# Kernel tuning notes

Measured on AMD Instinct MI355X. Metric: run time of the kernel, lower is better.

## Reference

```python
import jax, jax.numpy as jnp
import numpy as np

BN_EPS = 1e-5

def conv1d(x, w, b, pad):
    # x: (B, C_in, L), w: (C_out, C_in, K=4), stride 1
    y = jax.lax.conv_general_dilated(x, w, window_strides=(1,), padding=[(pad, pad)],
                                     dimension_numbers=('NCH', 'OIH', 'NCH'))
    return y + b[None, :, None]

def batchnorm_train(x, g, be):
    # training-mode BN over (N, L) per channel, biased variance (torch semantics)
    m = jnp.mean(x, axis=(0, 2), keepdims=True)
    v = jnp.mean((x - m) ** 2, axis=(0, 2), keepdims=True)
    return (x - m) * jax.lax.rsqrt(v + BN_EPS) * g[None, :, None] + be[None, :, None]

def setup_inputs() -> dict:
    key = jax.random.key(0)
    ks = jax.random.split(key, 12)
    B, T, C_in, E, K = 32, 4096, 12, 256, 1024
    d = {}
    d['x'] = jax.random.normal(ks[0], (B, T, C_in), jnp.float32)
    d['w1'] = jax.random.normal(ks[1], (E, C_in, 4), jnp.float32) * 0.1
    d['b1'] = jax.random.normal(ks[2], (E,), jnp.float32) * 0.1
    d['g1'] = jnp.ones((E,), jnp.float32); d['be1'] = jnp.zeros((E,), jnp.float32)
    d['w2'] = jax.random.normal(ks[3], (E, E, 4), jnp.float32) * 0.05
    d['b2'] = jax.random.normal(ks[4], (E,), jnp.float32) * 0.1
    d['g2'] = jnp.ones((E,), jnp.float32); d['be2'] = jnp.zeros((E,), jnp.float32)
    d['w3'] = jax.random.normal(ks[5], (E, E, 4), jnp.float32) * 0.05
    d['b3'] = jax.random.normal(ks[6], (E,), jnp.float32) * 0.1
    d['g3'] = jnp.ones((E,), jnp.float32); d['be3'] = jnp.zeros((E,), jnp.float32)
    d['w4'] = jax.random.normal(ks[7], (E, E, 4), jnp.float32) * 0.05
    d['b4'] = jax.random.normal(ks[8], (E,), jnp.float32) * 0.1
    d['codebook'] = jax.random.normal(ks[9], (K, E), jnp.float32)
    return d

def reference(x, w1, b1, g1, be1, w2, b2, g2, be2, w3, b3, g3, be3, w4, b4, codebook):
    h = jnp.transpose(x, (0, 2, 1))                 # (B, C, T)
    h = jax.nn.relu(batchnorm_train(conv1d(h, w1, b1, 2), g1, be1))  # (B,E,T+1)
    h = jax.nn.relu(batchnorm_train(conv1d(h, w2, b2, 1), g2, be2))  # (B,E,T)
    h = jax.nn.relu(batchnorm_train(conv1d(h, w3, b3, 2), g3, be3))  # (B,E,T+1)
    h = conv1d(h, w4, b4, 1)                                         # (B,E,T)
    z_e = jnp.transpose(h, (0, 2, 1))               # (B, T, E)
    # squared-L2 nearest codebook entry (argmin identical to cdist p=2)
    d2 = (jnp.sum(z_e ** 2, axis=-1, keepdims=True)
          - 2.0 * jnp.einsum('bte,ke->btk', z_e, codebook)
          + jnp.sum(codebook ** 2, axis=-1)[None, None, :])
    ids = jnp.argmin(d2, axis=-1)                   # (B, T) int
    z_q = codebook[ids]                             # gather (B, T, E)
    z_q = z_e + jax.lax.stop_gradient(z_q - z_e)    # straight-through
    return (z_e, z_q)
```

## Files before the change

kernel.cpp:

```cpp
#include <hip/hip_runtime.h>
#include <hip/hip_bf16.h>


#define B_   32
#define T_   4096
#define E_   256
#define CIN_ 12
#define LM_  4096

typedef __attribute__((ext_vector_type(4))) float f32x4;
typedef __attribute__((ext_vector_type(8))) short bf16x8;
typedef __attribute__((ext_vector_type(8))) unsigned short u16x8;

__device__ __forceinline__ unsigned int bf_rne(float v) {
  unsigned int u = __float_as_uint(v);
  return (u + 0x7fffu + ((u >> 16) & 1u)) >> 16;
}
__device__ __forceinline__ void split2(float v, unsigned short& h, unsigned short& l) {
  unsigned int hu = bf_rne(v);
  h = (unsigned short)hu;
  l = (unsigned short)bf_rne(v - __uint_as_float(hu << 16));
}
__device__ __forceinline__ void split3(float v, unsigned short& a,
                                       unsigned short& b, unsigned short& c) {
  unsigned int h = bf_rne(v);
  a = (unsigned short)h;
  float r1 = v - __uint_as_float(h << 16);
  unsigned int m = bf_rne(r1);
  b = (unsigned short)m;
  float r2 = r1 - __uint_as_float(m << 16);
  c = (unsigned short)bf_rne(r2);
}

__global__ __launch_bounds__(256) void prep_w_kernel(
    const float* __restrict__ w, unsigned short* __restrict__ wh,
    unsigned short* __restrict__ wm, unsigned short* __restrict__ wl) {
  const int g = blockIdx.x * 256 + threadIdx.x;
  const int coff  = g & 31;
  const int e     = (g >> 5) & 255;
  const int slice = g >> 13;
  const int cc = slice >> 2, kt = slice & 3;
  const int c = cc * 32 + coff;
  unsigned short h, m, l;
  split3(w[(size_t)e * 1024 + (size_t)c * 4 + kt], h, m, l);
  const size_t o = (size_t)slice * 8192 + (size_t)e * 32 + coff;
  wh[o] = h; wm[o] = m; wl[o] = l;
}

__global__ __launch_bounds__(256) void conv1_kernel(
    const float* __restrict__ x, const float* __restrict__ w1,
    const float* __restrict__ b1, float* __restrict__ out_main,
    float* __restrict__ out_tail) {
  __shared__ __align__(16) float xs[259][12];
  __shared__ __align__(16) float wsh[E_ * 48];
  __shared__ float bs[E_];
  const int tid = threadIdx.x;
  const int b = blockIdx.y;
  const int l0 = blockIdx.x * 256;
  for (int idx = tid; idx < 259 * 12; idx += 256) {
    int r = idx / 12, c = idx - r * 12;
    int t = l0 - 2 + r;
    xs[r][c] = (t >= 0 && t < T_) ? x[((size_t)b * T_ + t) * CIN_ + c] : 0.f;
  }
  for (int idx = tid; idx < E_ * 48; idx += 256) wsh[idx] = w1[idx];
  bs[tid] = b1[tid];
  __syncthreads();
  float xr[4][12];
  #pragma unroll
  for (int r = 0; r < 4; ++r)
    #pragma unroll
    for (int c = 0; c < 12; ++c) xr[r][c] = xs[tid + r][c];
  const int l = l0 + tid;
  for (int e = 0; e < E_; ++e) {
    float acc = bs[e];
    #pragma unroll
    for (int c = 0; c < 12; ++c) {
      const float4 wv = *(const float4*)&wsh[e * 48 + c * 4];
      acc += wv.x * xr[0][c] + wv.y * xr[1][c] + wv.z * xr[2][c] + wv.w * xr[3][c];
    }
    if (l < LM_)       out_main[((size_t)b * E_ + e) * LM_ + l] = acc;
    else if (l == LM_) out_tail[(size_t)b * E_ + e] = acc;
  }
}

__global__ __launch_bounds__(256) void bn_pass1(
    const float* __restrict__ hmain, const float* __restrict__ htail,
    float* __restrict__ psum, float* __restrict__ psq) {
  const int bx = blockIdx.x;
  const int c = bx >> 3, sl = bx & 7;
  const int tid = threadIdx.x;
  float s = 0.f, s2 = 0.f;
  for (int b = 0; b < B_; ++b) {
    const float* p = hmain + ((size_t)b * E_ + c) * LM_ + sl * 512;
    const float v0 = p[tid], v1 = p[tid + 256];
    s += v0 + v1;
    s2 += v0 * v0 + v1 * v1;
  }
  if (htail && sl == 7 && tid < B_) {
    const float v = htail[(size_t)tid * E_ + c];
    s += v; s2 += v * v;
  }
  __shared__ float sh[256], sh2[256];
  sh[tid] = s; sh2[tid] = s2; __syncthreads();
  for (int off = 128; off > 0; off >>= 1) {
    if (tid < off) { sh[tid] += sh[tid + off]; sh2[tid] += sh2[tid + off]; }
    __syncthreads();
  }
  if (tid == 0) { psum[bx] = sh[0]; psq[bx] = sh2[0]; }
}

__global__ __launch_bounds__(256) void bn_pass2(
    const float* __restrict__ psum, const float* __restrict__ psq,
    const float* __restrict__ g, const float* __restrict__ be,
    float* __restrict__ scale, float* __restrict__ shift, int hasTail) {
  const int c = threadIdx.x;
  double s = 0.0, s2 = 0.0;
  #pragma unroll
  for (int i = 0; i < 8; ++i) { s += psum[c * 8 + i]; s2 += psq[c * 8 + i]; }
  double N = (double)B_ * (double)(LM_ + hasTail);
  double m = s / N, var = s2 / N - m * m;
  double a = (double)g[c] / sqrt(var + 1e-5);
  scale[c] = (float)a;
  shift[c] = (float)((double)be[c] - m * a);
}

template <int MODE>
__global__ __launch_bounds__(256) void conv_mfma(
    const float* __restrict__ in_main, const float* __restrict__ in_tail,
    const unsigned short* __restrict__ wh, const unsigned short* __restrict__ wm,
    const unsigned short* __restrict__ wl, const float* __restrict__ bias,
    const float* __restrict__ scale, const float* __restrict__ shift,
    float* __restrict__ out, float* __restrict__ out_tail, int pad) {
  __shared__ __align__(16) char XhB[132 * 64];
  __shared__ __align__(16) char XmB[132 * 64];
  __shared__ __align__(16) char XlB[132 * 64];
  __shared__ float sc_sh[E_], sf_sh[E_];
  const int tid = threadIdx.x, lane = tid & 63, wv = tid >> 6;
  const int q = lane >> 4, n16 = lane & 15;
  const int b = blockIdx.z, e0 = blockIdx.y * 128, l0 = blockIdx.x * 128;
  const int eB = e0 + (wv & 1) * 64;
  const int lB = (wv >> 1) * 64;
  sc_sh[tid] = scale[tid]; sf_sh[tid] = shift[tid];

  f32x4 acc[4][4];
  #pragma unroll
  for (int i = 0; i < 4; ++i)
    #pragma unroll
    for (int j = 0; j < 4; ++j) acc[i][j] = (f32x4){0.f, 0.f, 0.f, 0.f};

  const float* inb = in_main + (size_t)b * E_ * LM_;
  const float* intb = in_tail ? (in_tail + (size_t)b * E_) : nullptr;

  for (int cc = 0; cc < 8; ++cc) {
    __syncthreads();
    for (int idx = tid; idx < 528; idx += 256) {
      const int cp = idx & 15, uq = idx >> 4;
      const int c = cc * 32 + cp * 2;
      const int u0 = uq * 4;
      const int lb = l0 - pad + u0;
      const float* pa = inb + (size_t)c * LM_;
      const float* pb = pa + LM_;
      const float sca = sc_sh[c], sfa = sf_sh[c];
      const float scb = sc_sh[c + 1], sfb = sf_sh[c + 1];
      float fa[4], fb[4];
      if (lb >= 0 && lb + 3 < LM_) {
        const f32x4 va = *(const f32x4*)(pa + lb);
        const f32x4 vb = *(const f32x4*)(pb + lb);
        #pragma unroll
        for (int s = 0; s < 4; ++s) {
          fa[s] = fmaxf(fmaf(va[s], sca, sfa), 0.f);
          fb[s] = fmaxf(fmaf(vb[s], scb, sfb), 0.f);
        }
      } else {
        #pragma unroll
        for (int s = 0; s < 4; ++s) {
          const int l = lb + s;
          float oa = 0.f, ob = 0.f;
          if (l >= 0 && l < LM_) {
            oa = fmaxf(fmaf(pa[l], sca, sfa), 0.f);
            ob = fmaxf(fmaf(pb[l], scb, sfb), 0.f);
          } else if (l == LM_ && intb) {
            oa = fmaxf(fmaf(intb[c], sca, sfa), 0.f);
            ob = fmaxf(fmaf(intb[c + 1], scb, sfb), 0.f);
          }
          fa[s] = oa; fb[s] = ob;
        }
      }
      const int cg = cp >> 2;
      const int cb4 = (cp & 3) * 4;
      #pragma unroll
      for (int s = 0; s < 4; ++s) {
        const int u = u0 + s;
        unsigned short ha, ma, la, hb, mb, lb2;
        split3(fa[s], ha, ma, la);
        split3(fb[s], hb, mb, lb2);
        const int off = u * 64 + ((cg ^ ((u >> 1) & 3)) << 4) + cb4;
        *(unsigned int*)(XhB + off) = (unsigned int)ha | ((unsigned int)hb << 16);
        *(unsigned int*)(XmB + off) = (unsigned int)ma | ((unsigned int)mb << 16);
        *(unsigned int*)(XlB + off) = (unsigned int)la | ((unsigned int)lb2 << 16);
      }
    }
    __syncthreads();
    for (int kt = 0; kt < 4; ++kt) {
      bf16x8 Bh[4], Bm[4], Bl[4];
      #pragma unroll
      for (int ni = 0; ni < 4; ++ni) {
        const int u = lB + ni * 16 + n16 + kt;
        const int off = u * 64 + ((q ^ ((u >> 1) & 3)) << 4);
        Bh[ni] = *(const bf16x8*)(XhB + off);
        Bm[ni] = *(const bf16x8*)(XmB + off);
        Bl[ni] = *(const bf16x8*)(XlB + off);
      }
      const size_t so = (size_t)(cc * 4 + kt) * 8192 + (size_t)q * 8;
      #pragma unroll
      for (int mi = 0; mi < 4; ++mi) {
        const size_t o = so + (size_t)(eB + mi * 16 + n16) * 32;
        const bf16x8 Ah = *(const bf16x8*)(wh + o);
        const bf16x8 Am = *(const bf16x8*)(wm + o);
        const bf16x8 Al = *(const bf16x8*)(wl + o);
        #pragma unroll
        for (int ni = 0; ni < 4; ++ni) {
          acc[mi][ni] = __builtin_amdgcn_mfma_f32_16x16x32_bf16(Ah, Bh[ni], acc[mi][ni], 0, 0, 0);
          acc[mi][ni] = __builtin_amdgcn_mfma_f32_16x16x32_bf16(Ah, Bm[ni], acc[mi][ni], 0, 0, 0);
          acc[mi][ni] = __builtin_amdgcn_mfma_f32_16x16x32_bf16(Am, Bh[ni], acc[mi][ni], 0, 0, 0);
          acc[mi][ni] = __builtin_amdgcn_mfma_f32_16x16x32_bf16(Ah, Bl[ni], acc[mi][ni], 0, 0, 0);
          acc[mi][ni] = __builtin_amdgcn_mfma_f32_16x16x32_bf16(Al, Bh[ni], acc[mi][ni], 0, 0, 0);
          acc[mi][ni] = __builtin_amdgcn_mfma_f32_16x16x32_bf16(Am, Bm[ni], acc[mi][ni], 0, 0, 0);
        }
      }
    }
  }

  #pragma unroll
  for (int mi = 0; mi < 4; ++mi) {
    const int eb4 = eB + mi * 16 + q * 4;
    const f32x4 bv = *(const f32x4*)(bias + eb4);
    #pragma unroll
    for (int ni = 0; ni < 4; ++ni) {
      const int col = l0 + lB + ni * 16 + n16;
      const f32x4 r = acc[mi][ni] + bv;
      if constexpr (MODE == 0) {
        #pragma unroll
        for (int rr = 0; rr < 4; ++rr)
          out[((size_t)b * E_ + eb4 + rr) * LM_ + col] = r[rr];
      } else if constexpr (MODE == 1) {
        if (col < LM_) {
          #pragma unroll
          for (int rr = 0; rr < 4; ++rr)
            out[((size_t)b * E_ + eb4 + rr) * LM_ + col] = r[rr];
        } else if (col == LM_) {
          #pragma unroll
          for (int rr = 0; rr < 4; ++rr)
            out_tail[(size_t)b * E_ + eb4 + rr] = r[rr];
        }
      } else {
        #pragma unroll
        for (int rr = 0; rr < 4; ++rr)
          out[((size_t)b * T_ + col) * E_ + eb4 + rr] = r[rr];
      }
    }
  }
}

__global__ __launch_bounds__(256) void cbprep_kernel(
    const float* __restrict__ cb, unsigned short* __restrict__ cbh,
    unsigned short* __restrict__ cbl, float* __restrict__ cnh) {
  const int code = blockIdx.x * 4 + (threadIdx.x >> 6);
  const int lane = threadIdx.x & 63;
  const f32x4 v = *(const f32x4*)&cb[(size_t)code * E_ + lane * 4];
  ushort4 h, l;
  split2(v.x, h.x, l.x); split2(v.y, h.y, l.y);
  split2(v.z, h.z, l.z); split2(v.w, h.w, l.w);
  *(ushort4*)&cbh[(size_t)code * E_ + lane * 4] = h;
  *(ushort4*)&cbl[(size_t)code * E_ + lane * 4] = l;
  float s = v.x * v.x + v.y * v.y + v.z * v.z + v.w * v.w;
  for (int off = 32; off > 0; off >>= 1) s += __shfl_xor(s, off, 64);
  if (lane == 0) cnh[code] = 0.5f * s;
}

__global__ __launch_bounds__(256) void vq_mfma_kernel(
    const float* __restrict__ z, const unsigned short* __restrict__ cbh,
    const unsigned short* __restrict__ cbl, const float* __restrict__ cnh,
    int* __restrict__ ids) {
  __shared__ __align__(16) char cbLds[2][16384];
  __shared__ float cn_sh[1024];
  const int tid = threadIdx.x;
  const int lane = tid & 63;
  const int w = tid >> 6;
  const int q = lane >> 4;
  const int m15 = lane & 15;
  const int rbase = blockIdx.x * 128 + w * 32;
  for (int i = tid; i < 1024; i += 256) cn_sh[i] = cnh[i];

  const int sc0 = tid >> 5, sl0 = tid & 31;
  const int sc1 = (tid + 256) >> 5, sl1 = (tid + 256) & 31;
  const int d0 = sc0 * 512 + (((sl0 ^ (sc0 & 7))) << 4);
  const int d1 = sc1 * 512 + (((sl1 ^ (sc1 & 7))) << 4);
  const u16x8* srcH = (const u16x8*)cbh;
  const u16x8* srcL = (const u16x8*)cbl;

  {
    u16x8 h0 = srcH[tid], h1 = srcH[tid + 256];
    u16x8 l0 = srcL[tid], l1 = srcL[tid + 256];
    *(u16x8*)(cbLds[0] + d0) = h0;
    *(u16x8*)(cbLds[0] + d1) = h1;
    *(u16x8*)(cbLds[0] + 8192 + d0) = l0;
    *(u16x8*)(cbLds[0] + 8192 + d1) = l1;
  }

  bf16x8 zh[2][8], zl[2][8];
  #pragma unroll
  for (int g = 0; g < 2; ++g) {
    const int row = rbase + g * 16 + m15;
    const float* zr = z + (size_t)row * 256 + q * 8;
    #pragma unroll
    for (int ec = 0; ec < 8; ++ec) {
      const f32x4 v0 = *(const f32x4*)(zr + ec * 32);
      const f32x4 v1 = *(const f32x4*)(zr + ec * 32 + 4);
      u16x8 h, l;
      #pragma unroll
      for (int j = 0; j < 4; ++j) {
        unsigned short a, b;
        split2(v0[j], a, b); h[j] = a; l[j] = b;
        split2(v1[j], a, b); h[4 + j] = a; l[4 + j] = b;
      }
      zh[g][ec] = (bf16x8)h;
      zl[g][ec] = (bf16x8)l;
    }
  }
  __syncthreads();

  float best[2] = {-3.4e38f, -3.4e38f};
  int bidx[2] = {0, 0};
  const int swz = (m15 & 7) << 4;
  const int rowOff = m15 * 512;

  for (int cg = 0; cg < 64; ++cg) {
    const int cur = cg & 1;
    u16x8 ph0, ph1, pl0, pl1;
    if (cg < 63) {
      const int sb = (cg + 1) * 512;
      ph0 = srcH[sb + tid]; ph1 = srcH[sb + tid + 256];
      pl0 = srcL[sb + tid]; pl1 = srcL[sb + tid + 256];
    }
    const char* baseH = cbLds[cur];
    const char* baseL = cbLds[cur] + 8192;
    f32x4 ahh[2], ahl[2], alh[2];
    #pragma unroll
    for (int g = 0; g < 2; ++g) {
      ahh[g] = (f32x4){0.f, 0.f, 0.f, 0.f};
      ahl[g] = (f32x4){0.f, 0.f, 0.f, 0.f};
      alh[g] = (f32x4){0.f, 0.f, 0.f, 0.f};
    }
    #pragma unroll
    for (int ec = 0; ec < 8; ++ec) {
      const int co = rowOff + ((q * 16 + ec * 64) ^ swz);
      const bf16x8 Ah = *(const bf16x8*)(baseH + co);
      const bf16x8 Al = *(const bf16x8*)(baseL + co);
      #pragma unroll
      for (int g = 0; g < 2; ++g) {
        ahh[g] = __builtin_amdgcn_mfma_f32_16x16x32_bf16(Ah, zh[g][ec], ahh[g], 0, 0, 0);
        ahl[g] = __builtin_amdgcn_mfma_f32_16x16x32_bf16(Ah, zl[g][ec], ahl[g], 0, 0, 0);
        alh[g] = __builtin_amdgcn_mfma_f32_16x16x32_bf16(Al, zh[g][ec], alh[g], 0, 0, 0);
      }
    }
    const f32x4 cn = *(const f32x4*)&cn_sh[cg * 16 + q * 4];
    #pragma unroll
    for (int g = 0; g < 2; ++g) {
      #pragma unroll
      for (int r = 0; r < 4; ++r) {
        const float s = (ahh[g][r] + ahl[g][r]) + alh[g][r] - cn[r];
        const int code = cg * 16 + q * 4 + r;
        if (s > best[g]) { best[g] = s; bidx[g] = code; }
      }
    }
    if (cg < 63) {
      char* nb = cbLds[cur ^ 1];
      *(u16x8*)(nb + d0) = ph0;
      *(u16x8*)(nb + d1) = ph1;
      *(u16x8*)(nb + 8192 + d0) = pl0;
      *(u16x8*)(nb + 8192 + d1) = pl1;
    }
    __syncthreads();
  }

  #pragma unroll
  for (int g = 0; g < 2; ++g) {
    #pragma unroll
    for (int off = 16; off <= 32; off <<= 1) {
      const float ov = __shfl_xor(best[g], off, 64);
      const int oi = __shfl_xor(bidx[g], off, 64);
      if (ov > best[g] || (ov == best[g] && oi < bidx[g])) { best[g] = ov; bidx[g] = oi; }
    }
  }
  if (q == 0) {
    #pragma unroll
    for (int g = 0; g < 2; ++g) ids[rbase + g * 16 + lane] = bidx[g];
  }
}

__global__ __launch_bounds__(256) void gather_kernel(
    const int* __restrict__ ids, const float* __restrict__ cb,
    float* __restrict__ zq) {
  const int row = blockIdx.x * 4 + (threadIdx.x >> 6);
  const int lane = threadIdx.x & 63;
  const int id = ids[row];
  const float4 v = *(const float4*)&cb[(size_t)id * E_ + lane * 4];
  *(float4*)&zq[(size_t)row * E_ + lane * 4] = v;
}

extern "C" void kernel_launch(void* const* d_in, const int* in_sizes, int n_in,
                              void* d_out, int out_size, void* d_ws, size_t ws_size,
                              hipStream_t stream) {
  const float* x   = (const float*)d_in[0];
  const float* w1  = (const float*)d_in[1];
  const float* b1  = (const float*)d_in[2];
  const float* g1  = (const float*)d_in[3];
  const float* be1 = (const float*)d_in[4];
  const float* w2  = (const float*)d_in[5];
  const float* b2  = (const float*)d_in[6];
  const float* g2  = (const float*)d_in[7];
  const float* be2 = (const float*)d_in[8];
  const float* w3  = (const float*)d_in[9];
  const float* b3  = (const float*)d_in[10];
  const float* g3  = (const float*)d_in[11];
  const float* be3 = (const float*)d_in[12];
  const float* w4  = (const float*)d_in[13];
  const float* b4  = (const float*)d_in[14];
  const float* cb  = (const float*)d_in[15];

  char* ws = (char*)d_ws;
  float* tailA  = (float*)(ws);
  float* scale1 = (float*)(ws + 40960);  float* shift1 = (float*)(ws + 45056);
  float* scale2 = (float*)(ws + 49152);  float* shift2 = (float*)(ws + 53248);
  float* scale3 = (float*)(ws + 57344);  float* shift3 = (float*)(ws + 61440);
  float* cnh    = (float*)(ws + 65536);
  float* psum   = (float*)(ws + 73728);
  float* psq    = (float*)(ws + 81920);
  int*   ids    = (int*)(ws + 131072);
  const size_t MB = 1u << 20;
  unsigned short* wh2 = (unsigned short*)(ws + MB);
  unsigned short* wm2 = (unsigned short*)(ws + MB + 524288u);
  unsigned short* wl2 = (unsigned short*)(ws + MB + 1048576u);
  unsigned short* wh3 = (unsigned short*)(ws + MB + 1572864u);
  unsigned short* wm3 = (unsigned short*)(ws + MB + 2097152u);
  unsigned short* wl3 = (unsigned short*)(ws + MB + 2621440u);
  unsigned short* wh4 = (unsigned short*)(ws + MB + 3145728u);
  unsigned short* wm4 = (unsigned short*)(ws + MB + 3670016u);
  unsigned short* wl4 = (unsigned short*)(ws + MB + 4194304u);

  float* half1 = (float*)d_out;
  float* half2 = half1 + (size_t)33554432;
  unsigned short* cbh = (unsigned short*)half2;
  unsigned short* cbl = (unsigned short*)half2 + 262144;

  prep_w_kernel<<<1024, 256, 0, stream>>>(w2, wh2, wm2, wl2);
  prep_w_kernel<<<1024, 256, 0, stream>>>(w3, wh3, wm3, wl3);
  prep_w_kernel<<<1024, 256, 0, stream>>>(w4, wh4, wm4, wl4);

  conv1_kernel<<<dim3(17, 32), 256, 0, stream>>>(x, w1, b1, half2, tailA);
  bn_pass1<<<2048, 256, 0, stream>>>(half2, tailA, psum, psq);
  bn_pass2<<<1, 256, 0, stream>>>(psum, psq, g1, be1, scale1, shift1, 1);
  conv_mfma<0><<<dim3(32, 2, 32), 256, 0, stream>>>(half2, tailA, wh2, wm2, wl2, b2,
                                                    scale1, shift1, half1, nullptr, 1);
  bn_pass1<<<2048, 256, 0, stream>>>(half1, nullptr, psum, psq);
  bn_pass2<<<1, 256, 0, stream>>>(psum, psq, g2, be2, scale2, shift2, 0);
  conv_mfma<1><<<dim3(33, 2, 32), 256, 0, stream>>>(half1, nullptr, wh3, wm3, wl3, b3,
                                                    scale2, shift2, half2, tailA, 2);
  bn_pass1<<<2048, 256, 0, stream>>>(half2, tailA, psum, psq);
  bn_pass2<<<1, 256, 0, stream>>>(psum, psq, g3, be3, scale3, shift3, 1);
  conv_mfma<2><<<dim3(32, 2, 32), 256, 0, stream>>>(half2, tailA, wh4, wm4, wl4, b4,
                                                    scale3, shift3, half1, nullptr, 1);
  cbprep_kernel<<<256, 256, 0, stream>>>(cb, cbh, cbl, cnh);
  vq_mfma_kernel<<<1024, 256, 0, stream>>>(half1, cbh, cbl, cnh, ids);
  gather_kernel<<<32768, 256, 0, stream>>>(ids, cb, half2);
}
```

Baseline: 1.462 ms.

## Double-buffer conv input tiles in LDS with register prefetch overlapping MFMA

```diff
diff --git a/kernel.cpp b/kernel.cpp
--- a/kernel.cpp
+++ b/kernel.cpp
@@ -131,9 +131,7 @@
     const unsigned short* __restrict__ wl, const float* __restrict__ bias,
     const float* __restrict__ scale, const float* __restrict__ shift,
     float* __restrict__ out, float* __restrict__ out_tail, int pad) {
-  __shared__ __align__(16) char XhB[132 * 64];
-  __shared__ __align__(16) char XmB[132 * 64];
-  __shared__ __align__(16) char XlB[132 * 64];
+  __shared__ __align__(16) char Xb[2][3][8448];
   __shared__ float sc_sh[E_], sf_sh[E_];
   const int tid = threadIdx.x, lane = tid & 63, wv = tid >> 6;
   const int q = lane >> 4, n16 = lane & 15;
@@ -151,56 +149,77 @@
   const float* inb = in_main + (size_t)b * E_ * LM_;
   const float* intb = in_tail ? (in_tail + (size_t)b * E_) : nullptr;
 
+  auto loadTask = [&](int idx, int cc, f32x4& va, f32x4& vb) {
+    const int cp = idx & 15, uq = idx >> 4;
+    const int c = cc * 32 + cp * 2;
+    const int u0 = uq * 4;
+    const int lb = l0 - pad + u0;
+    const float* pa = inb + (size_t)c * LM_;
+    const float* pb = pa + LM_;
+    if (lb >= 0 && lb + 3 < LM_) {
+      va = *(const f32x4*)(pa + lb);
+      vb = *(const f32x4*)(pb + lb);
+    } else {
+      #pragma unroll
+      for (int s = 0; s < 4; ++s) {
+        const int l = lb + s;
+        float oa = 0.f, ob = 0.f;
+        if (l >= 0 && l < LM_)        { oa = pa[l]; ob = pb[l]; }
+        else if (l == LM_ && intb)    { oa = intb[c]; ob = intb[c + 1]; }
+        va[s] = oa; vb[s] = ob;
+      }
+    }
+  };
+  auto writeTask = [&](int idx, int cc, f32x4 va, f32x4 vb, int nb) {
+    const int cp = idx & 15, uq = idx >> 4;
+    const int c = cc * 32 + cp * 2;
+    const int u0 = uq * 4;
+    const int lb = l0 - pad + u0;
+    const float sca = sc_sh[c], sfa = sf_sh[c];
+    const float scb = sc_sh[c + 1], sfb = sf_sh[c + 1];
+    const int cg = cp >> 2;
+    const int cb4 = (cp & 3) * 4;
+    #pragma unroll
+    for (int s = 0; s < 4; ++s) {
+      const int l = lb + s;
+      const bool ok = (l >= 0) && (l < LM_ || (l == LM_ && intb));
+      const float fa = ok ? fmaxf(fmaf(va[s], sca, sfa), 0.f) : 0.f;
+      const float fb = ok ? fmaxf(fmaf(vb[s], scb, sfb), 0.f) : 0.f;
+      unsigned short ha, ma, la, hb, mb, lb2;
+      split3(fa, ha, ma, la);
+      split3(fb, hb, mb, lb2);
+      const int u = u0 + s;
+      const int off = u * 64 + ((cg ^ ((u >> 1) & 3)) << 4) + cb4;
+      *(unsigned int*)(Xb[nb][0] + off) = (unsigned int)ha | ((unsigned int)hb << 16);
+      *(unsigned int*)(Xb[nb][1] + off) = (unsigned int)ma | ((unsigned int)mb << 16);
+      *(unsigned int*)(Xb[nb][2] + off) = (unsigned int)la | ((unsigned int)lb2 << 16);
+    }
+  };
+
+  __syncthreads();
+  {
+    f32x4 va, vb;
+    #pragma unroll
+    for (int s2 = 0; s2 < 3; ++s2) {
+      const int idx = tid + s2 * 256;
+      if (idx < 528) { loadTask(idx, 0, va, vb); writeTask(idx, 0, va, vb, 0); }
+    }
+  }
+  __syncthreads();
+
   for (int cc = 0; cc < 8; ++cc) {
-    __syncthreads();
-    for (int idx = tid; idx < 528; idx += 256) {
-      const int cp = idx & 15, uq = idx >> 4;
-      const int c = cc * 32 + cp * 2;
-      const int u0 = uq * 4;
-      const int lb = l0 - pad + u0;
-      const float* pa = inb + (size_t)c * LM_;
-      const float* pb = pa + LM_;
-      const float sca = sc_sh[c], sfa = sf_sh[c];
-      const float scb = sc_sh[c + 1], sfb = sf_sh[c + 1];
-      float fa[4], fb[4];
-      if (lb >= 0 && lb + 3 < LM_) {
-        const f32x4 va = *(const f32x4*)(pa + lb);
-        const f32x4 vb = *(const f32x4*)(pb + lb);
-        #pragma unroll
-        for (int s = 0; s < 4; ++s) {
-          fa[s] = fmaxf(fmaf(va[s], sca, sfa), 0.f);
-          fb[s] = fmaxf(fmaf(vb[s], scb, sfb), 0.f);
-        }
-      } else {
-        #pragma unroll
-        for (int s = 0; s < 4; ++s) {
-          const int l = lb + s;
-          float oa = 0.f, ob = 0.f;
-          if (l >= 0 && l < LM_) {
-            oa = fmaxf(fmaf(pa[l], sca, sfa), 0.f);
-            ob = fmaxf(fmaf(pb[l], scb, sfb), 0.f);
-          } else if (l == LM_ && intb) {
-            oa = fmaxf(fmaf(intb[c], sca, sfa), 0.f);
-            ob = fmaxf(fmaf(intb[c + 1], scb, sfb), 0.f);
-          }
-          fa[s] = oa; fb[s] = ob;
-        }
-      }
-      const int cg = cp >> 2;
-      const int cb4 = (cp & 3) * 4;
-      #pragma unroll
-      for (int s = 0; s < 4; ++s) {
-        const int u = u0 + s;
-        unsigned short ha, ma, la, hb, mb, lb2;
-        split3(fa[s], ha, ma, la);
-        split3(fb[s], hb, mb, lb2);
-        const int off = u * 64 + ((cg ^ ((u >> 1) & 3)) << 4) + cb4;
-        *(unsigned int*)(XhB + off) = (unsigned int)ha | ((unsigned int)hb << 16);
-        *(unsigned int*)(XmB + off) = (unsigned int)ma | ((unsigned int)mb << 16);
-        *(unsigned int*)(XlB + off) = (unsigned int)la | ((unsigned int)lb2 << 16);
-      }
-    }
-    __syncthreads();
+    const int cur = cc & 1;
+    f32x4 pva[3], pvb[3];
+    if (cc < 7) {
+      #pragma unroll
+      for (int s2 = 0; s2 < 3; ++s2) {
+        const int idx = tid + s2 * 256;
+        if (idx < 528) loadTask(idx, cc + 1, pva[s2], pvb[s2]);
+      }
+    }
+    const char* XhB = Xb[cur][0];
+    const char* XmB = Xb[cur][1];
+    const char* XlB = Xb[cur][2];
     for (int kt = 0; kt < 4; ++kt) {
       bf16x8 Bh[4], Bm[4], Bl[4];
       #pragma unroll
@@ -229,6 +248,14 @@
         }
       }
     }
+    if (cc < 7) {
+      #pragma unroll
+      for (int s2 = 0; s2 < 3; ++s2) {
+        const int idx = tid + s2 * 256;
+        if (idx < 528) writeTask(idx, cc + 1, pva[s2], pvb[s2], cur ^ 1);
+      }
+    }
+    __syncthreads();
   }
 
   #pragma unroll
```

After: 1.649 ms. 1.13x slower.
